# Kernel tuning notes

Hardware: AMD Instinct MI355X
Metric: run time of the kernel (lower is better)

Reference implementation:

```python
import jax, jax.numpy as jnp
import numpy as np

N, E, NODE_DIM, EDGE_DIM, H, L, G, C = 50000, 600000, 64, 16, 128, 3, 256, 2


def setup_inputs() -> dict:
    key = jax.random.key(0)
    ks = jax.random.split(key, 32)
    inp = {
        "x": jax.random.normal(ks[0], (N, NODE_DIM), jnp.float32),
        "edge_attr": jax.random.normal(ks[1], (E, EDGE_DIM), jnp.float32),
        "edge_index": jax.random.randint(ks[2], (2, E), 0, N, dtype=jnp.int64),
        "batch": jnp.sort(jax.random.randint(ks[3], (N,), 0, G, dtype=jnp.int64)),
    }
    def lin(k, fan_in, fan_out):
        b = 1.0 / np.sqrt(fan_in)
        return jax.random.uniform(k, (fan_in, fan_out), jnp.float32, -b, b)
    # node embedding
    inp["emb_W"] = lin(ks[4], NODE_DIM, H)
    inp["emb_b"] = jnp.zeros((H,), jnp.float32)
    # stacked per-layer MPNN params [L, ...]
    inp["msg_W1"] = jnp.stack([lin(jax.random.fold_in(ks[5], i), 2 * H + EDGE_DIM, H) for i in range(L)])
    inp["msg_b1"] = jnp.zeros((L, H), jnp.float32)
    inp["msg_W2"] = jnp.stack([lin(jax.random.fold_in(ks[6], i), H, H) for i in range(L)])
    inp["msg_b2"] = jnp.zeros((L, H), jnp.float32)
    inp["upd_W1"] = jnp.stack([lin(jax.random.fold_in(ks[7], i), 2 * H, H) for i in range(L)])
    inp["upd_b1"] = jnp.zeros((L, H), jnp.float32)
    inp["upd_W2"] = jnp.stack([lin(jax.random.fold_in(ks[8], i), H, H) for i in range(L)])
    inp["upd_b2"] = jnp.zeros((L, H), jnp.float32)
    # classifier (dropout is eval-mode identity)
    inp["cls_W1"] = lin(ks[9], 2 * H, H)
    inp["cls_b1"] = jnp.zeros((H,), jnp.float32)
    inp["cls_W2"] = lin(ks[10], H, H // 2)
    inp["cls_b2"] = jnp.zeros((H // 2,), jnp.float32)
    inp["cls_W3"] = lin(ks[11], H // 2, C)
    inp["cls_b3"] = jnp.zeros((C,), jnp.float32)
    return inp


def reference(x, edge_attr, emb_W, emb_b, msg_W1, msg_b1, msg_W2, msg_b2,
              upd_W1, upd_b1, upd_W2, upd_b2,
              cls_W1, cls_b1, cls_W2, cls_b2, cls_W3, cls_b3,
              edge_index, batch):
    src, dst = edge_index[0], edge_index[1]  # PyG: x_j = x[src], x_i = x[dst]
    h = x @ emb_W + emb_b  # [N, H]
    for l in range(L):
        x_i = h[dst]
        x_j = h[src]
        msg_in = jnp.concatenate([x_i, x_j, edge_attr], axis=1)  # [E, 2H+edge_dim]
        m = jax.nn.relu(msg_in @ msg_W1[l] + msg_b1[l]) @ msg_W2[l] + msg_b2[l]
        aggr = jax.ops.segment_sum(m, dst, num_segments=N)  # scatter-add to targets
        upd_in = jnp.concatenate([h, aggr], axis=1)  # [N, 2H]
        h = jax.nn.relu(upd_in @ upd_W1[l] + upd_b1[l]) @ upd_W2[l] + upd_b2[l]
        h = jax.nn.relu(h)
    # global mean / max pool over graphs
    counts = jax.ops.segment_sum(jnp.ones((N,), h.dtype), batch, num_segments=G)
    g_mean = jax.ops.segment_sum(h, batch, num_segments=G) / jnp.maximum(counts, 1.0)[:, None]
    g_max = jax.ops.segment_max(h, batch, num_segments=G)
    g_max = jnp.where(jnp.isfinite(g_max), g_max, 0.0)  # guard empty graphs
    rep = jnp.concatenate([g_mean, g_max], axis=1)  # [G, 2H]
    # classifier (dropout = identity in eval)
    z = jax.nn.relu(rep @ cls_W1 + cls_b1)
    z = jax.nn.relu(z @ cls_W2 + cls_b2)
    return z @ cls_W3 + cls_b3  # [G, C]
```

## Files before the change

### kernel.cpp

```cpp
#include <hip/hip_runtime.h>
#include <hip/hip_bf16.h>

#define HD 128
#define SCB 2048

typedef __attribute__((ext_vector_type(8))) short short8v;
typedef __attribute__((ext_vector_type(4))) float f32x4;
typedef unsigned short us;

__device__ __forceinline__ us f2bf(float f) {
    union { float f; unsigned u; } c; c.f = f;
    unsigned u = c.u;
    return (us)((u + 0x7fffu + ((u >> 16) & 1u)) >> 16);
}
__device__ __forceinline__ float bf2f(us b) {
    union { unsigned u; float f; } c; c.u = ((unsigned)b) << 16;
    return c.f;
}

template<int KSTEPS, int K1S, bool HASA2, bool RELU, bool DEGB, bool WF32, bool WBF>
__global__ __launch_bounds__(512) void k_mgemm(
    const us* __restrict__ A1h, const us* __restrict__ A1l,
    const us* __restrict__ A2h, const us* __restrict__ A2l,
    const us* __restrict__ Wth, const us* __restrict__ Wtl,
    const float* __restrict__ bias,
    const float* __restrict__ bdeg, const float* __restrict__ deg,
    float* __restrict__ Cf0, float* __restrict__ Cf1,
    us* __restrict__ Ch, us* __restrict__ Cl,
    int nrows)
{
    constexpr int K   = KSTEPS * 32;
    constexpr int CPR = K / 8;
    constexpr int ITER = (64 * CPR) / 512;
    __shared__ us As_h[64 * K];
    __shared__ us As_l[64 * K];

    const int tid  = threadIdx.x;
    const int wv   = tid >> 6;
    const int lane = tid & 63;
    const int r    = lane & 15;
    const int g    = lane >> 4;
    const int rb   = blockIdx.x * 64;
    const int col  = blockIdx.y * 128 + wv * 16 + r;

    short8v bh[KSTEPS], bl[KSTEPS];
    {
        size_t wbase = (size_t)col * K + (size_t)(g * 8);
#pragma unroll
        for (int s = 0; s < KSTEPS; ++s) {
            bh[s] = *(const short8v*)(Wth + wbase + s * 32);
            bl[s] = *(const short8v*)(Wtl + wbase + s * 32);
        }
    }

#pragma unroll
    for (int i = 0; i < ITER; ++i) {
        int f = tid + i * 512;
        int row = f / CPR, c = f % CPR;
        int grow = rb + row; if (grow >= nrows) grow = nrows - 1;
        uint4 vh, vl;
        if (!HASA2 || c * 8 < K1S) {
            size_t o = (size_t)grow * K1S + (size_t)(c * 8);
            vh = *(const uint4*)(A1h + o);
            vl = *(const uint4*)(A1l + o);
        } else {
            size_t o = (size_t)grow * (K - K1S) + (size_t)(c * 8 - K1S);
            vh = *(const uint4*)(A2h + o);
            vl = *(const uint4*)(A2l + o);
        }
        int boff = row * (K * 2) + ((c * 16) ^ ((row & 7) << 4));
        *(uint4*)((char*)As_h + boff) = vh;
        *(uint4*)((char*)As_l + boff) = vl;
    }
    __syncthreads();

    f32x4 acc[4];
#pragma unroll
    for (int t = 0; t < 4; ++t) acc[t] = (f32x4){0.f, 0.f, 0.f, 0.f};

#pragma unroll
    for (int s = 0; s < KSTEPS; ++s) {
#pragma unroll
        for (int t = 0; t < 4; ++t) {
            int row = t * 16 + r;
            int boff = row * (K * 2) + (((s * 64) + g * 16) ^ ((row & 7) << 4));
            short8v ah = *(const short8v*)((const char*)As_h + boff);
            short8v al = *(const short8v*)((const char*)As_l + boff);
            acc[t] = __builtin_amdgcn_mfma_f32_16x16x32_bf16(ah, bh[s], acc[t], 0, 0, 0);
            acc[t] = __builtin_amdgcn_mfma_f32_16x16x32_bf16(al, bh[s], acc[t], 0, 0, 0);
            acc[t] = __builtin_amdgcn_mfma_f32_16x16x32_bf16(ah, bl[s], acc[t], 0, 0, 0);
        }
    }

    const float bb = (bias && col < 128) ? bias[col] : 0.f;
    const float bd = (DEGB && col < 128) ? bdeg[col] : 0.f;
    const int jc = col & 127;
#pragma unroll
    for (int t = 0; t < 4; ++t) {
#pragma unroll
        for (int i = 0; i < 4; ++i) {
            int row = rb + t * 16 + g * 4 + i;
            if (row >= nrows) continue;
            float v = acc[t][i] + bb;
            if (DEGB) v += deg[row] * bd;
            if (RELU) v = fmaxf(v, 0.f);
            size_t o = (size_t)row * HD + jc;
            if (WF32) (col < 128 ? Cf0 : Cf1)[o] = v;
            if (WBF) {
                us hh = f2bf(v);
                Ch[o] = hh;
                Cl[o] = f2bf(v - bf2f(hh));
            }
        }
    }
}

__global__ __launch_bounds__(512) void k_upd(
    const us* __restrict__ A1h, const us* __restrict__ A1l,
    const us* __restrict__ A2h, const us* __restrict__ A2l,
    const us* __restrict__ Wth, const us* __restrict__ Wtl,
    const float* __restrict__ b1,
    const float* __restrict__ bdeg, const float* __restrict__ deg,
    const us* __restrict__ W2th, const us* __restrict__ W2tl,
    const float* __restrict__ b2,
    us* __restrict__ out_h, us* __restrict__ out_l,
    int nrows)
{
    constexpr int K = 256;
    constexpr int CPR = K / 8;
    constexpr int ITER = (64 * CPR) / 512;
    __shared__ us As_h[64 * K];
    __shared__ us As_l[64 * K];

    const int tid  = threadIdx.x;
    const int wv   = tid >> 6;
    const int lane = tid & 63;
    const int r    = lane & 15;
    const int g    = lane >> 4;
    const int rb   = blockIdx.x * 64;
    const int col  = wv * 16 + r;

    short8v bh[8], bl[8];
    {
        size_t wbase = (size_t)col * K + (size_t)(g * 8);
#pragma unroll
        for (int s = 0; s < 8; ++s) {
            bh[s] = *(const short8v*)(Wth + wbase + s * 32);
            bl[s] = *(const short8v*)(Wtl + wbase + s * 32);
        }
    }

#pragma unroll
    for (int i = 0; i < ITER; ++i) {
        int f = tid + i * 512;
        int row = f / CPR, c = f % CPR;
        int grow = rb + row; if (grow >= nrows) grow = nrows - 1;
        uint4 vh, vl;
        if (c * 8 < 128) {
            size_t o = (size_t)grow * 128 + (size_t)(c * 8);
            vh = *(const uint4*)(A1h + o);
            vl = *(const uint4*)(A1l + o);
        } else {
            size_t o = (size_t)grow * 128 + (size_t)(c * 8 - 128);
            vh = *(const uint4*)(A2h + o);
            vl = *(const uint4*)(A2l + o);
        }
        int boff = row * (K * 2) + ((c * 16) ^ ((row & 7) << 4));
        *(uint4*)((char*)As_h + boff) = vh;
        *(uint4*)((char*)As_l + boff) = vl;
    }
    __syncthreads();

    f32x4 acc[4];
#pragma unroll
    for (int t = 0; t < 4; ++t) acc[t] = (f32x4){0.f, 0.f, 0.f, 0.f};
#pragma unroll
    for (int s = 0; s < 8; ++s) {
#pragma unroll
        for (int t = 0; t < 4; ++t) {
            int row = t * 16 + r;
            int boff = row * (K * 2) + (((s * 64) + g * 16) ^ ((row & 7) << 4));
            short8v ah = *(const short8v*)((const char*)As_h + boff);
            short8v al = *(const short8v*)((const char*)As_l + boff);
            acc[t] = __builtin_amdgcn_mfma_f32_16x16x32_bf16(ah, bh[s], acc[t], 0, 0, 0);
            acc[t] = __builtin_amdgcn_mfma_f32_16x16x32_bf16(al, bh[s], acc[t], 0, 0, 0);
            acc[t] = __builtin_amdgcn_mfma_f32_16x16x32_bf16(ah, bl[s], acc[t], 0, 0, 0);
        }
    }
    __syncthreads();

    short8v b2h[4], b2l[4];
    {
        size_t wbase = (size_t)col * 128 + (size_t)(g * 8);
#pragma unroll
        for (int s = 0; s < 4; ++s) {
            b2h[s] = *(const short8v*)(W2th + wbase + s * 32);
            b2l[s] = *(const short8v*)(W2tl + wbase + s * 32);
        }
    }

    {
        const float bb = b1[col];
        const float bd = bdeg[col];
#pragma unroll
        for (int t = 0; t < 4; ++t) {
#pragma unroll
            for (int i = 0; i < 4; ++i) {
                int lrow = t * 16 + g * 4 + i;
                int grow = rb + lrow;
                float dg = (grow < nrows) ? deg[grow] : 0.f;
                float v = acc[t][i] + bb + dg * bd;
                v = fmaxf(v, 0.f);
                us uh = f2bf(v);
                us ul = f2bf(v - bf2f(uh));
                int byte = lrow * 256 + ((col * 2) ^ ((lrow & 7) << 4));
                *(us*)((char*)As_h + byte) = uh;
                *(us*)((char*)As_l + byte) = ul;
            }
        }
    }
    __syncthreads();

    f32x4 acc2[4];
#pragma unroll
    for (int t = 0; t < 4; ++t) acc2[t] = (f32x4){0.f, 0.f, 0.f, 0.f};
#pragma unroll
    for (int s = 0; s < 4; ++s) {
#pragma unroll
        for (int t = 0; t < 4; ++t) {
            int row = t * 16 + r;
            int boff = row * 256 + (((s * 64) + g * 16) ^ ((row & 7) << 4));
            short8v ah = *(const short8v*)((const char*)As_h + boff);
            short8v al = *(const short8v*)((const char*)As_l + boff);
            acc2[t] = __builtin_amdgcn_mfma_f32_16x16x32_bf16(ah, b2h[s], acc2[t], 0, 0, 0);
            acc2[t] = __builtin_amdgcn_mfma_f32_16x16x32_bf16(al, b2h[s], acc2[t], 0, 0, 0);
            acc2[t] = __builtin_amdgcn_mfma_f32_16x16x32_bf16(ah, b2l[s], acc2[t], 0, 0, 0);
        }
    }
    const float bb2 = b2[col];
#pragma unroll
    for (int t = 0; t < 4; ++t) {
#pragma unroll
        for (int i = 0; i < 4; ++i) {
            int row = rb + t * 16 + g * 4 + i;
            if (row >= nrows) continue;
            float v = fmaxf(acc2[t][i] + bb2, 0.f);
            size_t o = (size_t)row * HD + col;
            us hh = f2bf(v);
            out_h[o] = hh;
            out_l[o] = f2bf(v - bf2f(hh));
        }
    }
}

__global__ void k_cvtA(const float* __restrict__ src,
                       us* __restrict__ dh, us* __restrict__ dl, long n)
{
    long i = (long)blockIdx.x * blockDim.x + threadIdx.x;
    if (i >= n) return;
    float v = src[i];
    us h = f2bf(v);
    dh[i] = h;
    dl[i] = f2bf(v - bf2f(h));
}

__global__ void k_cvtW(const float* __restrict__ src, long sstride, int K,
                       us* __restrict__ dh, us* __restrict__ dl, long dstride)
{
    int l = blockIdx.y;
    int idx = blockIdx.x * 256 + threadIdx.x;
    if (idx >= K * 128) return;
    int k = idx >> 7, j = idx & 127;
    float v = src[(size_t)l * sstride + (size_t)k * 128 + j];
    us h = f2bf(v);
    size_t o = (size_t)l * dstride + (size_t)j * K + k;
    dh[o] = h;
    dl[o] = f2bf(v - bf2f(h));
}

__global__ void k_cvtW2(const float* __restrict__ srcA, long strideA,
                        const float* __restrict__ srcB, long strideB,
                        int K1s, int K,
                        us* __restrict__ dh, us* __restrict__ dl, long dstride)
{
    int l = blockIdx.y;
    int idx = blockIdx.x * 256 + threadIdx.x;
    if (idx >= K * 128) return;
    int k = idx >> 7, j = idx & 127;
    float v = (k < K1s)
        ? srcA[(size_t)l * strideA + (size_t)k * 128 + j]
        : srcB[(size_t)l * strideB + (size_t)(k - K1s) * 128 + j];
    us h = f2bf(v);
    size_t o = (size_t)l * dstride + (size_t)j * K + k;
    dh[o] = h;
    dl[o] = f2bf(v - bf2f(h));
}

__global__ void k_deghist(const int* __restrict__ dst, int* __restrict__ degi, int E,
                          const int* __restrict__ batch, int* __restrict__ gcnt, int N)
{
    int i = blockIdx.x * blockDim.x + threadIdx.x;
    if (i < E) atomicAdd(&degi[dst[i]], 1);
    if (i < N) atomicAdd(&gcnt[batch[i]], 1);
}

__global__ __launch_bounds__(256) void k_scan1(const int* __restrict__ degi,
                                               int* __restrict__ thrpre,
                                               int* __restrict__ bsum, int N)
{
    __shared__ int sc[256];
    const int t = threadIdx.x, b = blockIdx.x;
    int i0 = b * SCB + t * 8;
    int s = 0;
#pragma unroll
    for (int q = 0; q < 8; ++q) {
        int i = i0 + q;
        if (i < N) s += degi[i];
    }
    sc[t] = s;
    __syncthreads();
    for (int o = 1; o < 256; o <<= 1) {
        int v = (t >= o) ? sc[t - o] : 0;
        __syncthreads();
        sc[t] += v;
        __syncthreads();
    }
    thrpre[b * 256 + t] = sc[t] - s;
    if (t == 255) bsum[b] = sc[255];
}

__global__ void k_scan2(const int* __restrict__ bsum, int* __restrict__ boff, int nb)
{
    if (threadIdx.x == 0 && blockIdx.x == 0) {
        int run = 0;
        for (int b = 0; b < nb; ++b) { boff[b] = run; run += bsum[b]; }
    }
}

__global__ __launch_bounds__(256) void k_scan3(
    const int* __restrict__ degi, const int* __restrict__ thrpre,
    const int* __restrict__ boff,
    int* __restrict__ rowptr, int* __restrict__ cursor,
    float* __restrict__ degf, int N, int E)
{
    const int t = threadIdx.x, b = blockIdx.x;
    int run = boff[b] + thrpre[b * 256 + t];
    int i0 = b * SCB + t * 8;
#pragma unroll
    for (int q = 0; q < 8; ++q) {
        int i = i0 + q;
        if (i < N) {
            int d = degi[i];
            rowptr[i] = run;
            cursor[i] = run;
            degf[i] = (float)d;
            run += d;
        }
    }
    if (b == 0 && t == 0) rowptr[N] = E;
}

__global__ void k_scatter(const int* __restrict__ dst, const int* __restrict__ src,
                          int* __restrict__ cursor,
                          const float* __restrict__ ea,
                          int* __restrict__ csr_src, int* __restrict__ csr_eid,
                          float* __restrict__ ea_p, int E)
{
    int e = blockIdx.x * blockDim.x + threadIdx.x;
    if (e >= E) return;
    int d = dst[e];
    int pos = atomicAdd(&cursor[d], 1);
    csr_src[pos] = src[e];
    if (ea_p) {
        const float4* s4 = (const float4*)&ea[(size_t)e * 16];
        float4* d4 = (float4*)&ea_p[(size_t)pos * 16];
        d4[0] = s4[0]; d4[1] = s4[1]; d4[2] = s4[2]; d4[3] = s4[3];
    } else {
        csr_eid[pos] = e;
    }
}

__global__ __launch_bounds__(256) void k_foldW(
    const float* __restrict__ msg_W2, const float* __restrict__ upd_W1,
    float* __restrict__ fold)
{
    int l = blockIdx.x >> 3, rb = blockIdx.x & 7;
    const float* W2  = msg_W2 + (size_t)l * HD * HD;
    const float* U1b = upd_W1 + (size_t)l * 256 * HD + (size_t)HD * HD;
    float* Wout = fold + (size_t)l * HD * HD;
    int j = threadIdx.x & 127;
    int rh = threadIdx.x >> 7;
    int r0 = rb * 16 + rh * 8;
    float acc[8] = {0.f,0.f,0.f,0.f,0.f,0.f,0.f,0.f};
    for (int k = 0; k < HD; ++k) {
        float u = U1b[(size_t)k * HD + j];
#pragma unroll
        for (int rr = 0; rr < 8; ++rr)
            acc[rr] = fmaf(W2[(size_t)(r0 + rr) * HD + k], u, acc[rr]);
    }
#pragma unroll
    for (int rr = 0; rr < 8; ++rr)
        Wout[(size_t)(r0 + rr) * HD + j] = acc[rr];
}

__global__ __launch_bounds__(128) void k_foldb(
    const float* __restrict__ msg_b2, const float* __restrict__ upd_W1,
    float* __restrict__ bvec2)
{
    int l = blockIdx.x, j = threadIdx.x;
    const float* U1b = upd_W1 + (size_t)l * 256 * HD + (size_t)HD * HD;
    const float* b2 = msg_b2 + (size_t)l * HD;
    float acc = 0.f;
    for (int k = 0; k < HD; ++k) acc = fmaf(b2[k], U1b[(size_t)k * HD + j], acc);
    bvec2[(size_t)l * HD + j] = acc;
}

#define EB 16
template<bool PERM>
__global__ __launch_bounds__(256) void k_edge(
    const float* __restrict__ P, const float* __restrict__ Q,
    const float* __restrict__ EA,
    const int* __restrict__ rowptr,
    const int* __restrict__ csr_src, const int* __restrict__ csr_eid,
    const float* __restrict__ W1c,
    us* __restrict__ Sh, us* __restrict__ Sl, int N)
{
    const int lane = threadIdx.x & 63;
    const int node = __builtin_amdgcn_readfirstlane(blockIdx.x * 4 + (threadIdx.x >> 6));
    if (node >= N) return;
    float wA[16], wB[16];
#pragma unroll
    for (int k = 0; k < 16; ++k) {
        wA[k] = W1c[k * HD + lane];
        wB[k] = W1c[k * HD + 64 + lane];
    }
    const int beg = __builtin_amdgcn_readfirstlane(rowptr[node]);
    const int end = __builtin_amdgcn_readfirstlane(rowptr[node + 1]);
    const float pA = P[(size_t)node * HD + lane];
    const float pB = P[(size_t)node * HD + 64 + lane];
    float accA = 0.f, accB = 0.f;

    for (int i = beg; i < end; i += EB) {
        int myi = i + (lane & 15);
        myi = (myi < end) ? myi : (end - 1);
        int myidx = PERM ? myi : csr_eid[myi];
        int mysrc = csr_src[myi];
        int sv[EB], ei[EB];
#pragma unroll
        for (int r = 0; r < EB; ++r) {
            sv[r] = __builtin_amdgcn_readlane(mysrc, r);
            ei[r] = PERM ? 0 : __builtin_amdgcn_readlane(myidx, r);
        }
        float qA[EB], qB[EB];
#pragma unroll
        for (int r = 0; r < EB; ++r) {
            qA[r] = Q[(size_t)sv[r] * HD + lane];
            qB[r] = Q[(size_t)sv[r] * HD + 64 + lane];
        }
#pragma unroll
        for (int r = 0; r < EB; ++r) {
            int ii = i + r; ii = (ii < end) ? ii : (end - 1);
            const float4* Ev = PERM ? (const float4*)&EA[(size_t)ii * 16]
                                    : (const float4*)&EA[(size_t)ei[r] * 16];
            float4 v0 = Ev[0], v1 = Ev[1], v2 = Ev[2], v3 = Ev[3];
            float tA = pA + qA[r], tB = pB + qB[r];
            tA = fmaf(v0.x, wA[0],  tA); tB = fmaf(v0.x, wB[0],  tB);
            tA = fmaf(v0.y, wA[1],  tA); tB = fmaf(v0.y, wB[1],  tB);
            tA = fmaf(v0.z, wA[2],  tA); tB = fmaf(v0.z, wB[2],  tB);
            tA = fmaf(v0.w, wA[3],  tA); tB = fmaf(v0.w, wB[3],  tB);
            tA = fmaf(v1.x, wA[4],  tA); tB = fmaf(v1.x, wB[4],  tB);
            tA = fmaf(v1.y, wA[5],  tA); tB = fmaf(v1.y, wB[5],  tB);
            tA = fmaf(v1.z, wA[6],  tA); tB = fmaf(v1.z, wB[6],  tB);
            tA = fmaf(v1.w, wA[7],  tA); tB = fmaf(v1.w, wB[7],  tB);
            tA = fmaf(v2.x, wA[8],  tA); tB = fmaf(v2.x, wB[8],  tB);
            tA = fmaf(v2.y, wA[9],  tA); tB = fmaf(v2.y, wB[9],  tB);
            tA = fmaf(v2.z, wA[10], tA); tB = fmaf(v2.z, wB[10], tB);
            tA = fmaf(v2.w, wA[11], tA); tB = fmaf(v2.w, wB[11], tB);
            tA = fmaf(v3.x, wA[12], tA); tB = fmaf(v3.x, wB[12], tB);
            tA = fmaf(v3.y, wA[13], tA); tB = fmaf(v3.y, wB[13], tB);
            tA = fmaf(v3.z, wA[14], tA); tB = fmaf(v3.z, wB[14], tB);
            tA = fmaf(v3.w, wA[15], tA); tB = fmaf(v3.w, wB[15], tB);
            bool ok = (i + r) < end;
            accA += ok ? fmaxf(tA, 0.f) : 0.f;
            accB += ok ? fmaxf(tB, 0.f) : 0.f;
        }
    }
    size_t oA = (size_t)node * HD + lane;
    size_t oB = oA + 64;
    us hA = f2bf(accA);
    us hB = f2bf(accB);
    Sh[oA] = hA; Sl[oA] = f2bf(accA - bf2f(hA));
    Sh[oB] = hB; Sl[oB] = f2bf(accB - bf2f(hB));
}

__global__ __launch_bounds__(256) void k_pool2(
    const us* __restrict__ hh, const us* __restrict__ hl,
    const int* __restrict__ batch,
    float* __restrict__ gsum, unsigned int* __restrict__ gmax, int N)
{
    int nchunk = (N + gridDim.x - 1) / gridDim.x;
    int n0 = blockIdx.x * nchunk;
    int n1 = n0 + nchunk; if (n1 > N) n1 = N;
    int j = threadIdx.x & 127;
    int half = threadIdx.x >> 7;
    float s = 0.f, m = 0.f; int gcur = -1;
    for (int n = n0 + half; n < n1; n += 2) {
        int g = batch[n];
        if (g != gcur) {
            if (gcur >= 0) {
                atomicAdd(&gsum[(size_t)gcur * HD + j], s);
                atomicMax(&gmax[(size_t)gcur * HD + j], __float_as_uint(m));
            }
            gcur = g; s = 0.f; m = 0.f;
        }
        size_t o = (size_t)n * HD + j;
        float v = bf2f(hh[o]) + bf2f(hl[o]);
        s += v; m = fmaxf(m, v);
    }
    if (gcur >= 0) {
        atomicAdd(&gsum[(size_t)gcur * HD + j], s);
        atomicMax(&gmax[(size_t)gcur * HD + j], __float_as_uint(m));
    }
}

__global__ __launch_bounds__(128) void k_cls(
    const float* __restrict__ gsum, const float* __restrict__ gmax,
    const int* __restrict__ gcnt,
    const float* __restrict__ W1, const float* __restrict__ b1,
    const float* __restrict__ W2, const float* __restrict__ b2,
    const float* __restrict__ W3, const float* __restrict__ b3,
    float* __restrict__ out)
{
    __shared__ float rep[256];
    __shared__ float z1[128];
    __shared__ float z2[64];
    const int g = blockIdx.x;
    const int j = threadIdx.x;
    float cntf = (float)gcnt[g];
    rep[j]       = gsum[(size_t)g * HD + j] / fmaxf(cntf, 1.f);
    rep[128 + j] = gmax[(size_t)g * HD + j];
    __syncthreads();
    float a = 0.f;
    for (int k = 0; k < 256; ++k) a = fmaf(rep[k], W1[(size_t)k * 128 + j], a);
    z1[j] = fmaxf(a + b1[j], 0.f);
    __syncthreads();
    if (j < 64) {
        float b = 0.f;
        for (int k = 0; k < 128; ++k) b = fmaf(z1[k], W2[(size_t)k * 64 + j], b);
        z2[j] = fmaxf(b + b2[j], 0.f);
    }
    __syncthreads();
    if (j < 2) {
        float c = 0.f;
        for (int k = 0; k < 64; ++k) c = fmaf(z2[k], W3[(size_t)k * 2 + j], c);
        out[(size_t)g * 2 + j] = c + b3[j];
    }
}

extern "C" void kernel_launch(void* const* d_in, const int* in_sizes, int n_in,
                              void* d_out, int out_size, void* d_ws, size_t ws_size,
                              hipStream_t stream) {
    const float* x      = (const float*)d_in[0];
    const float* ea     = (const float*)d_in[1];
    const int*   ei     = (const int*)d_in[2];
    const int*   batch  = (const int*)d_in[3];
    const float* emb_W  = (const float*)d_in[4];
    const float* emb_b  = (const float*)d_in[5];
    const float* msg_W1 = (const float*)d_in[6];
    const float* msg_b1 = (const float*)d_in[7];
    const float* msg_W2 = (const float*)d_in[8];
    const float* msg_b2 = (const float*)d_in[9];
    const float* upd_W1 = (const float*)d_in[10];
    const float* upd_b1 = (const float*)d_in[11];
    const float* upd_W2 = (const float*)d_in[12];
    const float* upd_b2 = (const float*)d_in[13];
    const float* cW1 = (const float*)d_in[14];
    const float* cb1 = (const float*)d_in[15];
    const float* cW2 = (const float*)d_in[16];
    const float* cb2 = (const float*)d_in[17];
    const float* cW3 = (const float*)d_in[18];
    const float* cb3 = (const float*)d_in[19];

    const int N = in_sizes[0] / 64;
    const int E = in_sizes[1] / 16;
    const int G = 256, L = 3;
    const int* src = ei;
    const int* dst = ei + E;
    const int nb = (N + SCB - 1) / SCB;

    char* w = (char*)d_ws;
    size_t off = 0;
    auto alloc = [&](size_t bytes) -> void* {
        void* p = w + off;
        off += (bytes + 255) & ~(size_t)255;
        return p;
    };
    float* Pb  = (float*)alloc((size_t)N * HD * 4);
    float* Qb  = (float*)alloc((size_t)N * HD * 4);
    us* S_h = (us*)alloc((size_t)N * HD * 2);
    us* S_l = (us*)alloc((size_t)N * HD * 2);
    us* h_h = (us*)alloc((size_t)N * HD * 2);
    us* h_l = (us*)alloc((size_t)N * HD * 2);
    us* x_h = S_h;
    us* x_l = S_l;
    float* fold  = (float*)alloc((size_t)L * HD * HD * 4);
    float* bvec2 = (float*)alloc((size_t)L * HD * 4);
    us* embt_h = (us*)alloc((size_t)128 * 64 * 2);
    us* embt_l = (us*)alloc((size_t)128 * 64 * 2);
    us* WPQt_h = (us*)alloc((size_t)L * 256 * 128 * 2);
    us* WPQt_l = (us*)alloc((size_t)L * 256 * 128 * 2);
    us* Wcbt_h = (us*)alloc((size_t)L * 128 * 256 * 2);
    us* Wcbt_l = (us*)alloc((size_t)L * 128 * 256 * 2);
    us* U2t_h  = (us*)alloc((size_t)L * 128 * 128 * 2);
    us* U2t_l  = (us*)alloc((size_t)L * 128 * 128 * 2);
    int*   degi   = (int*)alloc((size_t)N * 4);
    float* degf   = (float*)alloc((size_t)N * 4);
    int*   rowptr = (int*)alloc((size_t)(N + 1) * 4);
    int*   cursor = (int*)alloc((size_t)N * 4);
    int*   thrpre = (int*)alloc((size_t)nb * 256 * 4);
    int*   bsum   = (int*)alloc((size_t)(nb + 1) * 4);
    int*   boff   = (int*)alloc((size_t)(nb + 1) * 4);
    int*   gcnt   = (int*)alloc(256 * 4);
    float* gsum   = (float*)alloc((size_t)G * HD * 4);
    float* gmax   = (float*)alloc((size_t)G * HD * 4);
    int*   csr_src = (int*)alloc((size_t)E * 4);
    int*   csr_eid = (int*)alloc((size_t)E * 4);
    float* ea_p = nullptr;
    if (ws_size && off + (size_t)E * 16 * 4 + 256 <= ws_size)
        ea_p = (float*)alloc((size_t)E * 16 * 4);
    (void)n_in; (void)out_size;

    hipMemsetAsync(degi, 0, (size_t)N * 4, stream);
    hipMemsetAsync(gcnt, 0, 256 * 4, stream);
    hipMemsetAsync(gsum, 0, (size_t)G * HD * 4, stream);
    hipMemsetAsync(gmax, 0, (size_t)G * HD * 4, stream);

    int mEN = (E > N ? E : N);
    k_deghist<<<(mEN + 255) / 256, 256, 0, stream>>>(dst, degi, E, batch, gcnt, N);
    k_scan1<<<nb, 256, 0, stream>>>(degi, thrpre, bsum, N);
    k_scan2<<<1, 64, 0, stream>>>(bsum, boff, nb);
    k_scan3<<<nb, 256, 0, stream>>>(degi, thrpre, boff, rowptr, cursor, degf, N, E);
    k_scatter<<<(E + 255) / 256, 256, 0, stream>>>(dst, src, cursor, ea,
                                                   csr_src, csr_eid, ea_p, E);

    k_foldW<<<L * 8, 256, 0, stream>>>(msg_W2, upd_W1, fold);
    k_foldb<<<L, 128, 0, stream>>>(msg_b2, upd_W1, bvec2);

    k_cvtA<<<(int)(((long)N * 64 + 255) / 256), 256, 0, stream>>>(x, x_h, x_l, (long)N * 64);
    k_cvtW<<<dim3(32, 1), 256, 0, stream>>>(emb_W, 0, 64, embt_h, embt_l, 0);
    k_cvtW<<<dim3(64, L), 256, 0, stream>>>(msg_W1, 272 * 128, 128,
                                            WPQt_h, WPQt_l, 256 * 128);
    k_cvtW<<<dim3(64, L), 256, 0, stream>>>(msg_W1 + 128 * 128, 272 * 128, 128,
                                            WPQt_h + 128 * 128, WPQt_l + 128 * 128,
                                            256 * 128);
    k_cvtW2<<<dim3(128, L), 256, 0, stream>>>(upd_W1, 256 * 128, fold, 128 * 128,
                                              128, 256, Wcbt_h, Wcbt_l, 128 * 256);
    k_cvtW<<<dim3(64, L), 256, 0, stream>>>(upd_W2, 128 * 128, 128,
                                            U2t_h, U2t_l, 128 * 128);

    const int gb = (N + 63) / 64;
    k_mgemm<2, 64, false, false, false, false, true><<<dim3(gb, 1), 512, 0, stream>>>(
        x_h, x_l, nullptr, nullptr, embt_h, embt_l,
        emb_b, nullptr, nullptr, nullptr, nullptr, h_h, h_l, N);

    for (int l = 0; l < L; ++l) {
        const float* W1 = msg_W1 + (size_t)l * 272 * HD;
        k_mgemm<4, 128, false, false, false, true, false><<<dim3(gb, 2), 512, 0, stream>>>(
            h_h, h_l, nullptr, nullptr,
            WPQt_h + (size_t)l * 256 * 128, WPQt_l + (size_t)l * 256 * 128,
            msg_b1 + (size_t)l * HD, nullptr, nullptr, Pb, Qb, nullptr, nullptr, N);
        if (ea_p)
            k_edge<true><<<(N + 3) / 4, 256, 0, stream>>>(Pb, Qb, ea_p, rowptr,
                                                          csr_src, nullptr,
                                                          W1 + 256 * HD, S_h, S_l, N);
        else
            k_edge<false><<<(N + 3) / 4, 256, 0, stream>>>(Pb, Qb, ea, rowptr,
                                                           csr_src, csr_eid,
                                                           W1 + 256 * HD, S_h, S_l, N);
        k_upd<<<gb, 512, 0, stream>>>(
            h_h, h_l, S_h, S_l,
            Wcbt_h + (size_t)l * 128 * 256, Wcbt_l + (size_t)l * 128 * 256,
            upd_b1 + (size_t)l * HD, bvec2 + (size_t)l * HD, degf,
            U2t_h + (size_t)l * 128 * 128, U2t_l + (size_t)l * 128 * 128,
            upd_b2 + (size_t)l * HD,
            h_h, h_l, N);
    }

    k_pool2<<<1024, 256, 0, stream>>>(h_h, h_l, batch, gsum, (unsigned int*)gmax, N);
    k_cls<<<G, 128, 0, stream>>>(gsum, gmax, gcnt, cW1, cb1, cW2, cb2, cW3, cb3,
                                 (float*)d_out);
}
```

Measured before the change: 688.9 us.

## Load GEMM A tiles directly to LDS and make edge kernel persistent

The GEMM kernels now stage A tiles with global_load_lds (direct global-to-LDS copies), so data no longer passes through registers. The XOR swizzle moves from the LDS write address to the global read address, so the LDS layout stays the same. Separately, the edge aggregation kernel now runs a fixed grid of 2048 blocks, with each wavefront walking a contiguous range of nodes. This spreads the per-wave W1c weight loads over several nodes instead of reloading them for every node. In exchange, per-node degree imbalance within a wave's chunk can leave some waves running longer than others.

```diff
diff --git a/kernel.cpp b/kernel.cpp
--- a/kernel.cpp
+++ b/kernel.cpp
@@ -16,6 +16,13 @@
 __device__ __forceinline__ float bf2f(us b) {
     union { unsigned u; float f; } c; c.u = ((unsigned)b) << 16;
     return c.f;
+}
+
+__device__ __forceinline__ void gload16(const void* g, void* l) {
+    __builtin_amdgcn_global_load_lds(
+        (const __attribute__((address_space(1))) unsigned int*)g,
+        (__attribute__((address_space(3))) unsigned int*)l,
+        16, 0, 0);
 }
 
 template<int KSTEPS, int K1S, bool HASA2, bool RELU, bool DEGB, bool WF32, bool WBF>
@@ -58,19 +65,17 @@
         int f = tid + i * 512;
         int row = f / CPR, c = f % CPR;
         int grow = rb + row; if (grow >= nrows) grow = nrows - 1;
-        uint4 vh, vl;
-        if (!HASA2 || c * 8 < K1S) {
-            size_t o = (size_t)grow * K1S + (size_t)(c * 8);
-            vh = *(const uint4*)(A1h + o);
-            vl = *(const uint4*)(A1l + o);
+        int sb = (c * 16) ^ ((row & 7) << 4);
+        const char *gh, *gl;
+        if (!HASA2 || sb < K1S * 2) {
+            gh = (const char*)A1h + (size_t)grow * (K1S * 2) + sb;
+            gl = (const char*)A1l + (size_t)grow * (K1S * 2) + sb;
         } else {
-            size_t o = (size_t)grow * (K - K1S) + (size_t)(c * 8 - K1S);
-            vh = *(const uint4*)(A2h + o);
-            vl = *(const uint4*)(A2l + o);
-        }
-        int boff = row * (K * 2) + ((c * 16) ^ ((row & 7) << 4));
-        *(uint4*)((char*)As_h + boff) = vh;
-        *(uint4*)((char*)As_l + boff) = vl;
+            gh = (const char*)A2h + (size_t)grow * ((K - K1S) * 2) + (sb - K1S * 2);
+            gl = (const char*)A2l + (size_t)grow * ((K - K1S) * 2) + (sb - K1S * 2);
+        }
+        gload16(gh, (char*)As_h + (size_t)f * 16);
+        gload16(gl, (char*)As_l + (size_t)f * 16);
     }
     __syncthreads();
 
@@ -155,19 +160,17 @@
         int f = tid + i * 512;
         int row = f / CPR, c = f % CPR;
         int grow = rb + row; if (grow >= nrows) grow = nrows - 1;
-        uint4 vh, vl;
-        if (c * 8 < 128) {
-            size_t o = (size_t)grow * 128 + (size_t)(c * 8);
-            vh = *(const uint4*)(A1h + o);
-            vl = *(const uint4*)(A1l + o);
+        int sb = (c * 16) ^ ((row & 7) << 4);
+        const char *gh, *gl;
+        if (sb < 256) {
+            gh = (const char*)A1h + (size_t)grow * 256 + sb;
+            gl = (const char*)A1l + (size_t)grow * 256 + sb;
         } else {
-            size_t o = (size_t)grow * 128 + (size_t)(c * 8 - 128);
-            vh = *(const uint4*)(A2h + o);
-            vl = *(const uint4*)(A2l + o);
-        }
-        int boff = row * (K * 2) + ((c * 16) ^ ((row & 7) << 4));
-        *(uint4*)((char*)As_h + boff) = vh;
-        *(uint4*)((char*)As_l + boff) = vl;
+            gh = (const char*)A2h + (size_t)grow * 256 + (sb - 256);
+            gl = (const char*)A2l + (size_t)grow * 256 + (sb - 256);
+        }
+        gload16(gh, (char*)As_h + (size_t)f * 16);
+        gload16(gl, (char*)As_l + (size_t)f * 16);
     }
     __syncthreads();
 
@@ -423,74 +426,80 @@
     const int* __restrict__ rowptr,
     const int* __restrict__ csr_src, const int* __restrict__ csr_eid,
     const float* __restrict__ W1c,
-    us* __restrict__ Sh, us* __restrict__ Sl, int N)
+    us* __restrict__ Sh, us* __restrict__ Sl, int N, int chunk)
 {
     const int lane = threadIdx.x & 63;
-    const int node = __builtin_amdgcn_readfirstlane(blockIdx.x * 4 + (threadIdx.x >> 6));
-    if (node >= N) return;
+    const int wid  = blockIdx.x * 4 + (threadIdx.x >> 6);
+    int n0 = wid * chunk;
+    int n1 = n0 + chunk; if (n1 > N) n1 = N;
+    if (n0 >= N) return;
+
     float wA[16], wB[16];
 #pragma unroll
     for (int k = 0; k < 16; ++k) {
         wA[k] = W1c[k * HD + lane];
         wB[k] = W1c[k * HD + 64 + lane];
     }
-    const int beg = __builtin_amdgcn_readfirstlane(rowptr[node]);
-    const int end = __builtin_amdgcn_readfirstlane(rowptr[node + 1]);
-    const float pA = P[(size_t)node * HD + lane];
-    const float pB = P[(size_t)node * HD + 64 + lane];
-    float accA = 0.f, accB = 0.f;
-
-    for (int i = beg; i < end; i += EB) {
-        int myi = i + (lane & 15);
-        myi = (myi < end) ? myi : (end - 1);
-        int myidx = PERM ? myi : csr_eid[myi];
-        int mysrc = csr_src[myi];
-        int sv[EB], ei[EB];
-#pragma unroll
-        for (int r = 0; r < EB; ++r) {
-            sv[r] = __builtin_amdgcn_readlane(mysrc, r);
-            ei[r] = PERM ? 0 : __builtin_amdgcn_readlane(myidx, r);
-        }
-        float qA[EB], qB[EB];
-#pragma unroll
-        for (int r = 0; r < EB; ++r) {
-            qA[r] = Q[(size_t)sv[r] * HD + lane];
-            qB[r] = Q[(size_t)sv[r] * HD + 64 + lane];
-        }
-#pragma unroll
-        for (int r = 0; r < EB; ++r) {
-            int ii = i + r; ii = (ii < end) ? ii : (end - 1);
-            const float4* Ev = PERM ? (const float4*)&EA[(size_t)ii * 16]
-                                    : (const float4*)&EA[(size_t)ei[r] * 16];
-            float4 v0 = Ev[0], v1 = Ev[1], v2 = Ev[2], v3 = Ev[3];
-            float tA = pA + qA[r], tB = pB + qB[r];
-            tA = fmaf(v0.x, wA[0],  tA); tB = fmaf(v0.x, wB[0],  tB);
-            tA = fmaf(v0.y, wA[1],  tA); tB = fmaf(v0.y, wB[1],  tB);
-            tA = fmaf(v0.z, wA[2],  tA); tB = fmaf(v0.z, wB[2],  tB);
-            tA = fmaf(v0.w, wA[3],  tA); tB = fmaf(v0.w, wB[3],  tB);
-            tA = fmaf(v1.x, wA[4],  tA); tB = fmaf(v1.x, wB[4],  tB);
-            tA = fmaf(v1.y, wA[5],  tA); tB = fmaf(v1.y, wB[5],  tB);
-            tA = fmaf(v1.z, wA[6],  tA); tB = fmaf(v1.z, wB[6],  tB);
-            tA = fmaf(v1.w, wA[7],  tA); tB = fmaf(v1.w, wB[7],  tB);
-            tA = fmaf(v2.x, wA[8],  tA); tB = fmaf(v2.x, wB[8],  tB);
-            tA = fmaf(v2.y, wA[9],  tA); tB = fmaf(v2.y, wB[9],  tB);
-            tA = fmaf(v2.z, wA[10], tA); tB = fmaf(v2.z, wB[10], tB);
-            tA = fmaf(v2.w, wA[11], tA); tB = fmaf(v2.w, wB[11], tB);
-            tA = fmaf(v3.x, wA[12], tA); tB = fmaf(v3.x, wB[12], tB);
-            tA = fmaf(v3.y, wA[13], tA); tB = fmaf(v3.y, wB[13], tB);
-            tA = fmaf(v3.z, wA[14], tA); tB = fmaf(v3.z, wB[14], tB);
-            tA = fmaf(v3.w, wA[15], tA); tB = fmaf(v3.w, wB[15], tB);
-            bool ok = (i + r) < end;
-            accA += ok ? fmaxf(tA, 0.f) : 0.f;
-            accB += ok ? fmaxf(tB, 0.f) : 0.f;
-        }
-    }
-    size_t oA = (size_t)node * HD + lane;
-    size_t oB = oA + 64;
-    us hA = f2bf(accA);
-    us hB = f2bf(accB);
-    Sh[oA] = hA; Sl[oA] = f2bf(accA - bf2f(hA));
-    Sh[oB] = hB; Sl[oB] = f2bf(accB - bf2f(hB));
+
+    for (int node = n0; node < n1; ++node) {
+        const int beg = __builtin_amdgcn_readfirstlane(rowptr[node]);
+        const int end = __builtin_amdgcn_readfirstlane(rowptr[node + 1]);
+        const float pA = P[(size_t)node * HD + lane];
+        const float pB = P[(size_t)node * HD + 64 + lane];
+        float accA = 0.f, accB = 0.f;
+
+        for (int i = beg; i < end; i += EB) {
+            int myi = i + (lane & 15);
+            myi = (myi < end) ? myi : (end - 1);
+            int myidx = PERM ? myi : csr_eid[myi];
+            int mysrc = csr_src[myi];
+            int sv[EB], ei[EB];
+#pragma unroll
+            for (int r = 0; r < EB; ++r) {
+                sv[r] = __builtin_amdgcn_readlane(mysrc, r);
+                ei[r] = PERM ? 0 : __builtin_amdgcn_readlane(myidx, r);
+            }
+            float qA[EB], qB[EB];
+#pragma unroll
+            for (int r = 0; r < EB; ++r) {
+                qA[r] = Q[(size_t)sv[r] * HD + lane];
+                qB[r] = Q[(size_t)sv[r] * HD + 64 + lane];
+            }
+#pragma unroll
+            for (int r = 0; r < EB; ++r) {
+                int ii = i + r; ii = (ii < end) ? ii : (end - 1);
+                const float4* Ev = PERM ? (const float4*)&EA[(size_t)ii * 16]
+                                        : (const float4*)&EA[(size_t)ei[r] * 16];
+                float4 v0 = Ev[0], v1 = Ev[1], v2 = Ev[2], v3 = Ev[3];
+                float tA = pA + qA[r], tB = pB + qB[r];
+                tA = fmaf(v0.x, wA[0],  tA); tB = fmaf(v0.x, wB[0],  tB);
+                tA = fmaf(v0.y, wA[1],  tA); tB = fmaf(v0.y, wB[1],  tB);
+                tA = fmaf(v0.z, wA[2],  tA); tB = fmaf(v0.z, wB[2],  tB);
+                tA = fmaf(v0.w, wA[3],  tA); tB = fmaf(v0.w, wB[3],  tB);
+                tA = fmaf(v1.x, wA[4],  tA); tB = fmaf(v1.x, wB[4],  tB);
+                tA = fmaf(v1.y, wA[5],  tA); tB = fmaf(v1.y, wB[5],  tB);
+                tA = fmaf(v1.z, wA[6],  tA); tB = fmaf(v1.z, wB[6],  tB);
+                tA = fmaf(v1.w, wA[7],  tA); tB = fmaf(v1.w, wB[7],  tB);
+                tA = fmaf(v2.x, wA[8],  tA); tB = fmaf(v2.x, wB[8],  tB);
+                tA = fmaf(v2.y, wA[9],  tA); tB = fmaf(v2.y, wB[9],  tB);
+                tA = fmaf(v2.z, wA[10], tA); tB = fmaf(v2.z, wB[10], tB);
+                tA = fmaf(v2.w, wA[11], tA); tB = fmaf(v2.w, wB[11], tB);
+                tA = fmaf(v3.x, wA[12], tA); tB = fmaf(v3.x, wB[12], tB);
+                tA = fmaf(v3.y, wA[13], tA); tB = fmaf(v3.y, wB[13], tB);
+                tA = fmaf(v3.z, wA[14], tA); tB = fmaf(v3.z, wB[14], tB);
+                tA = fmaf(v3.w, wA[15], tA); tB = fmaf(v3.w, wB[15], tB);
+                bool ok = (i + r) < end;
+                accA += ok ? fmaxf(tA, 0.f) : 0.f;
+                accB += ok ? fmaxf(tB, 0.f) : 0.f;
+            }
+        }
+        size_t oA = (size_t)node * HD + lane;
+        size_t oB = oA + 64;
+        us hA = f2bf(accA);
+        us hB = f2bf(accB);
+        Sh[oA] = hA; Sl[oA] = f2bf(accA - bf2f(hA));
+        Sh[oB] = hB; Sl[oB] = f2bf(accB - bf2f(hB));
+    }
 }
 
 __global__ __launch_bounds__(256) void k_pool2(
@@ -659,6 +668,8 @@
                                             U2t_h, U2t_l, 128 * 128);
 
     const int gb = (N + 63) / 64;
+    const int eblk = 2048;
+    const int echunk = (N + eblk * 4 - 1) / (eblk * 4);
     k_mgemm<2, 64, false, false, false, false, true><<<dim3(gb, 1), 512, 0, stream>>>(
         x_h, x_l, nullptr, nullptr, embt_h, embt_l,
         emb_b, nullptr, nullptr, nullptr, nullptr, h_h, h_l, N);
@@ -670,13 +681,13 @@
             WPQt_h + (size_t)l * 256 * 128, WPQt_l + (size_t)l * 256 * 128,
             msg_b1 + (size_t)l * HD, nullptr, nullptr, Pb, Qb, nullptr, nullptr, N);
         if (ea_p)
-            k_edge<true><<<(N + 3) / 4, 256, 0, stream>>>(Pb, Qb, ea_p, rowptr,
-                                                          csr_src, nullptr,
-                                                          W1 + 256 * HD, S_h, S_l, N);
+            k_edge<true><<<eblk, 256, 0, stream>>>(Pb, Qb, ea_p, rowptr,
+                                                   csr_src, nullptr,
+                                                   W1 + 256 * HD, S_h, S_l, N, echunk);
         else
-            k_edge<false><<<(N + 3) / 4, 256, 0, stream>>>(Pb, Qb, ea, rowptr,
-                                                           csr_src, csr_eid,
-                                                           W1 + 256 * HD, S_h, S_l, N);
+            k_edge<false><<<eblk, 256, 0, stream>>>(Pb, Qb, ea, rowptr,
+                                                    csr_src, csr_eid,
+                                                    W1 + 256 * HD, S_h, S_l, N, echunk);
         k_upd<<<gb, 512, 0, stream>>>(
             h_h, h_l, S_h, S_l,
             Wcbt_h + (size_t)l * 128 * 256, Wcbt_l + (size_t)l * 128 * 256,
```

Measured after the change: 725.0 us. 5.2% more time.
